# Optimization experiments

Measured on AMD Instinct MI355X. Metric: run time of the kernel, lower is better.

Reference implementation:

```python
import jax, jax.numpy as jnp
import numpy as np
import math

B, S, DM, L = 4, 512, 768, 2
DI, DS, K = 2 * DM, 16, 4          # mamba_ssm defaults: expand=2, d_state=16, d_conv=4
DTR = math.ceil(DM / 16)           # dt_rank = 48
F = 1


def setup_inputs() -> dict:
    key = jax.random.key(0)
    ks = iter(jax.random.split(key, 16))
    g = lambda shape, s=0.02: jax.random.normal(next(ks), shape, jnp.float32) * s
    # sinusoidal positional encoding (precomputed buffer)
    pos = np.arange(S)[:, None].astype(np.float32)
    div = np.exp(np.arange(0, DM, 2).astype(np.float32) * (-math.log(10000.0) / DM))
    pe = np.zeros((S, DM), np.float32)
    pe[:, 0::2] = np.sin(pos * div)
    pe[:, 1::2] = np.cos(pos * div)
    # S4D-real style A init
    A_log = jnp.broadcast_to(jnp.log(jnp.arange(1, DS + 1, dtype=jnp.float32)), (L, DI, DS))
    return dict(
        x=jax.random.normal(next(ks), (B, S, F), jnp.float32),
        w_in=g((DM, F)), b_in=jnp.zeros((DM,), jnp.float32),
        pe=jnp.asarray(pe)[None],                       # (1, S, DM)
        ln1_w=jnp.ones((L, DM)), ln1_b=jnp.zeros((L, DM)),
        w_inproj=g((L, 2 * DI, DM)),
        conv_w=g((L, DI, K), 0.1), conv_b=jnp.zeros((L, DI)),
        w_xproj=g((L, DTR + 2 * DS, DI)),
        w_dt=g((L, DI, DTR)), b_dt=jnp.full((L, DI), -4.0, jnp.float32),
        A_log=A_log, D=jnp.ones((L, DI)),
        w_outproj=g((L, DM, DI)),
        ln2_w=jnp.ones((L, DM)), ln2_b=jnp.zeros((L, DM)),
        ff_w1=g((L, 2 * DM, DM)), ff_b1=jnp.zeros((L, 2 * DM)),
        ff_w2=g((L, DM, 2 * DM)), ff_b2=jnp.zeros((L, DM)),
        lnf_w=jnp.ones((DM,)), lnf_b=jnp.zeros((DM,)),
        w_head=g((1, DM)), b_head=jnp.zeros((1,), jnp.float32),
    )


def _ln(x, w, b):
    mu = x.mean(-1, keepdims=True)
    v = ((x - mu) ** 2).mean(-1, keepdims=True)
    return (x - mu) * jax.lax.rsqrt(v + 1e-5) * w + b


def _mamba(x, w_inproj, conv_w, conv_b, w_xproj, w_dt, b_dt, A_log, D_, w_outproj):
    # x: (B, S, DM)
    Bsz = x.shape[0]
    xz = jnp.einsum('bsd,ed->bse', x, w_inproj)         # (B, S, 2*DI)
    xm, z = jnp.split(xz, 2, axis=-1)
    # causal depthwise conv1d over time
    xc = jax.lax.conv_general_dilated(
        xm.transpose(0, 2, 1), conv_w[:, None, :], (1,), [(K - 1, 0)],
        feature_group_count=DI, dimension_numbers=('NCH', 'OIH', 'NCH'))
    xc = jax.nn.silu((xc + conv_b[:, None]).transpose(0, 2, 1))  # (B, S, DI)
    dbc = jnp.einsum('bsd,ed->bse', xc, w_xproj)        # (B, S, DTR+2*DS)
    dt, Bm, Cm = dbc[..., :DTR], dbc[..., DTR:DTR + DS], dbc[..., DTR + DS:]
    delta = jax.nn.softplus(jnp.einsum('bsr,dr->bsd', dt, w_dt) + b_dt)  # (B, S, DI)
    A = -jnp.exp(A_log)                                 # (DI, DS)

    def step(h, inp):
        d_t, B_t, C_t, u_t = inp                        # (B,DI),(B,DS),(B,DS),(B,DI)
        h = h * jnp.exp(d_t[:, :, None] * A) + (d_t * u_t)[:, :, None] * B_t[:, None, :]
        return h, jnp.einsum('bds,bs->bd', h, C_t)

    h0 = jnp.zeros((Bsz, DI, DS), x.dtype)
    _, ys = jax.lax.scan(step, h0, (delta.transpose(1, 0, 2), Bm.transpose(1, 0, 2),
                                    Cm.transpose(1, 0, 2), xc.transpose(1, 0, 2)))
    y = ys.transpose(1, 0, 2) + xc * D_
    y = y * jax.nn.silu(z)
    return jnp.einsum('bsd,ed->bse', y, w_outproj)


def reference(x, w_in, b_in, pe, ln1_w, ln1_b, w_inproj, conv_w, conv_b, w_xproj,
              w_dt, b_dt, A_log, D, w_outproj, ln2_w, ln2_b, ff_w1, ff_b1,
              ff_w2, ff_b2, lnf_w, lnf_b, w_head, b_head):
    h = jnp.einsum('bsf,df->bsd', x, w_in) + b_in
    h = h + pe[:, :h.shape[1]]
    for l in range(L):  # fixed small layer count
        h = h + _mamba(_ln(h, ln1_w[l], ln1_b[l]), w_inproj[l], conv_w[l], conv_b[l],
                       w_xproj[l], w_dt[l], b_dt[l], A_log[l], D[l], w_outproj[l])
        f = _ln(h, ln2_w[l], ln2_b[l])
        f = jax.nn.gelu(jnp.einsum('bsd,ed->bse', f, ff_w1[l]) + ff_b1[l], approximate=False)
        h = h + jnp.einsum('bse,de->bsd', f, ff_w2[l]) + ff_b2[l]
    h = _ln(h, lnf_w, lnf_b)
    h = h.mean(axis=1)                                  # mean pool over time
    return jnp.einsum('bd,od->bo', h, w_head) + b_head
```

## Files before the change

kernel.cpp:

```cpp
#include <hip/hip_runtime.h>
#include <hip/hip_bf16.h>
#include <math.h>

#define B_ 4
#define S_ 512
#define DM_ 768
#define L_ 2
#define DI_ 1536
#define DS_ 16
#define KC_ 4
#define DTR_ 48
#define NSEG 8
#define TS 64

typedef __hip_bfloat16 bf16;
typedef __attribute__((ext_vector_type(8))) short short8;
typedef __attribute__((ext_vector_type(4))) float f32x4;

#define GLDS16(g, l) __builtin_amdgcn_global_load_lds( \
    (const __attribute__((address_space(1))) void*)(g), \
    (__attribute__((address_space(3))) void*)(l), 16, 0, 0)


__global__ void k_embed(const float* __restrict__ x, const float* __restrict__ w_in,
                        const float* __restrict__ b_in, const float* __restrict__ pe,
                        float* __restrict__ h) {
  int idx = blockIdx.x * 256 + threadIdx.x;
  if (idx >= B_ * S_ * DM_) return;
  int d = idx % DM_;
  int t = idx / DM_;
  int s = t % S_;
  h[idx] = x[t] * w_in[d] + b_in[d] + pe[s * DM_ + d];
}

__global__ void k_ln(const float* __restrict__ in, const float* __restrict__ w,
                     const float* __restrict__ b, bf16* __restrict__ out) {
  __shared__ float red1[4], red2[4];
  __shared__ float s_mu, s_rstd;
  int row = blockIdx.x;
  const float* x = in + (size_t)row * DM_;
  float s1 = 0.f, s2 = 0.f;
  for (int i = threadIdx.x; i < DM_; i += 256) { float v = x[i]; s1 += v; s2 += v * v; }
  for (int off = 32; off; off >>= 1) { s1 += __shfl_down(s1, off); s2 += __shfl_down(s2, off); }
  if ((threadIdx.x & 63) == 0) { red1[threadIdx.x >> 6] = s1; red2[threadIdx.x >> 6] = s2; }
  __syncthreads();
  if (threadIdx.x == 0) {
    float t1 = red1[0] + red1[1] + red1[2] + red1[3];
    float t2 = red2[0] + red2[1] + red2[2] + red2[3];
    float mu = t1 * (1.f / DM_);
    float var = t2 * (1.f / DM_) - mu * mu;
    s_mu = mu;
    s_rstd = rsqrtf(var + 1e-5f);
  }
  __syncthreads();
  float mu = s_mu, rstd = s_rstd;
  for (int i = threadIdx.x; i < DM_; i += 256)
    out[(size_t)row * DM_ + i] = __float2bfloat16((x[i] - mu) * rstd * w[i] + b[i]);
}

__global__ __launch_bounds__(256)
void k_lnred(const float* __restrict__ pxp, int KS,
             const float* __restrict__ hin, const float* __restrict__ bias,
             const float* __restrict__ lw, const float* __restrict__ lb,
             float* __restrict__ hout, bf16* __restrict__ xout) {
  __shared__ float red1[4], red2[4];
  __shared__ float s_mu, s_rstd;
  int row = blockIdx.x;
  float v[3];
  float s1 = 0.f, s2 = 0.f;
#pragma unroll
  for (int j = 0; j < 3; ++j) {
    int n = threadIdx.x + j * 256;
    float s = hin[(size_t)row * DM_ + n];
    if (bias) s += bias[n];
    for (int ks = 0; ks < KS; ++ks)
      s += pxp[(size_t)ks * 2048 * DM_ + (size_t)row * DM_ + n];
    v[j] = s;
    s1 += s; s2 += s * s;
  }
  for (int off = 32; off; off >>= 1) { s1 += __shfl_down(s1, off); s2 += __shfl_down(s2, off); }
  if ((threadIdx.x & 63) == 0) { red1[threadIdx.x >> 6] = s1; red2[threadIdx.x >> 6] = s2; }
  __syncthreads();
  if (threadIdx.x == 0) {
    float t1 = red1[0] + red1[1] + red1[2] + red1[3];
    float t2 = red2[0] + red2[1] + red2[2] + red2[3];
    float mu = t1 * (1.f / DM_);
    float var = t2 * (1.f / DM_) - mu * mu;
    s_mu = mu;
    s_rstd = rsqrtf(var + 1e-5f);
  }
  __syncthreads();
  float mu = s_mu, rstd = s_rstd;
#pragma unroll
  for (int j = 0; j < 3; ++j) {
    int n = threadIdx.x + j * 256;
    hout[(size_t)row * DM_ + n] = v[j];
    xout[(size_t)row * DM_ + n] = __float2bfloat16((v[j] - mu) * rstd * lw[n] + lb[n]);
  }
}

__global__ void k_gelred(const float* __restrict__ pxp, const float* __restrict__ bias,
                         bf16* __restrict__ out) {
  int idx = blockIdx.x * 256 + threadIdx.x;
  if (idx >= 2048 * 2 * DM_) return;
  int n = idx % (2 * DM_);
  float s = pxp[idx] + pxp[(size_t)2048 * 2 * DM_ + idx] + bias[n];
  s = 0.5f * s * (1.f + erff(s * 0.70710678118654752f));
  out[idx] = __float2bfloat16(s);
}

__global__ void k_castall(const float* __restrict__ w_inproj, const float* __restrict__ w_outproj,
                          const float* __restrict__ ff_w1, const float* __restrict__ ff_w2,
                          const float* __restrict__ w_xproj, const float* __restrict__ w_dt,
                          const float* __restrict__ A_log,
                          bf16* __restrict__ wip, bf16* __restrict__ wop,
                          bf16* __restrict__ wf1, bf16* __restrict__ wf2,
                          bf16* __restrict__ wxp, bf16* __restrict__ wdtp,
                          float* __restrict__ At) {
  const int N0 = L_ * 2 * DI_ * DM_;
  const int N1 = L_ * DM_ * DI_;
  const int N2 = L_ * 2 * DM_ * DM_;
  const int N3 = L_ * DM_ * 2 * DM_;
  const int N4 = L_ * 128 * DI_;
  const int N5 = L_ * DI_ * 64;
  const int N6 = L_ * 16 * DI_;
  const int TOT = N0 + N1 + N2 + N3 + N4 + N5 + N6;
  for (int i = blockIdx.x * 256 + threadIdx.x; i < TOT; i += gridDim.x * 256) {
    int j = i;
    if (j < N0) { wip[j] = __float2bfloat16(w_inproj[j]); continue; }
    j -= N0;
    if (j < N1) { wop[j] = __float2bfloat16(w_outproj[j]); continue; }
    j -= N1;
    if (j < N2) { wf1[j] = __float2bfloat16(ff_w1[j]); continue; }
    j -= N2;
    if (j < N3) { wf2[j] = __float2bfloat16(ff_w2[j]); continue; }
    j -= N3;
    if (j < N4) {
      int col = j % DI_;
      int row = (j / DI_) & 127;
      int l = j / (128 * DI_);
      float v = (row < 80) ? w_xproj[((size_t)l * 80 + row) * DI_ + col] : 0.f;
      wxp[j] = __float2bfloat16(v);
      continue;
    }
    j -= N4;
    if (j < N5) {
      int col = j & 63;
      int r = (j >> 6) % DI_;
      int l = j / (DI_ * 64);
      float v = (col < 48) ? w_dt[((size_t)l * DI_ + r) * 48 + col] : 0.f;
      wdtp[j] = __float2bfloat16(v);
      continue;
    }
    j -= N5;
    {
      int d = j % DI_;
      int n = (j / DI_) & 15;
      int l = j / (16 * DI_);
      At[j] = -__expf(A_log[((size_t)l * DI_ + d) * 16 + n]);
    }
  }
}

__global__ void k_conv_silu(const float* __restrict__ xz, const float* __restrict__ cw,
                            const float* __restrict__ cb, float* __restrict__ xc,
                            bf16* __restrict__ xcb) {
  int idx = blockIdx.x * 256 + threadIdx.x;
  if (idx >= B_ * S_ * DI_) return;
  int d = idx % DI_;
  int t = idx / DI_;
  int s = t % S_;
  int b = t / S_;
  float acc = cb[d];
  const float* base = xz + (size_t)(b * S_) * (2 * DI_) + d;
#pragma unroll
  for (int k = 0; k < KC_; ++k) {
    int ss = s - (KC_ - 1) + k;
    if (ss >= 0) acc = fmaf(base[(size_t)ss * (2 * DI_)], cw[d * KC_ + k], acc);
  }
  float v = acc / (1.f + expf(-acc));
  xc[idx] = v;
  xcb[idx] = __float2bfloat16(v);
}

__global__ __launch_bounds__(256)
void k_scanA(const float* __restrict__ delta, const float* __restrict__ xc,
             const float* __restrict__ bc, const float* __restrict__ At,
             const float* __restrict__ Dv,
             float* __restrict__ ylocal, float* __restrict__ cumd,
             float* __restrict__ hend) {
  int b = blockIdx.y;
  int seg = blockIdx.z;
  int d = blockIdx.x * 256 + threadIdx.x;
  int s0 = seg * TS;

  float A[16], hst[16];
#pragma unroll
  for (int n = 0; n < 16; ++n) {
    A[n] = At[(size_t)n * DI_ + d];
    hst[n] = 0.f;
  }
  float Dd = Dv[d];
  float cd = 0.f;

  const float* dp = delta + ((size_t)(b * S_ + s0)) * DI_ + d;
  const float* up = xc + ((size_t)(b * S_ + s0)) * DI_ + d;
  const float* bp = bc + ((size_t)(b * S_ + s0)) * 32;
  float* yp = ylocal + ((size_t)(b * S_ + s0)) * DI_ + d;
  float* cp = cumd + ((size_t)(b * S_ + s0)) * DI_ + d;

  float dl_next = dp[0];
  float u_next = up[0];
#pragma unroll 4
  for (int s = 0; s < TS; ++s) {
    float dl = dl_next, u = u_next;
    if (s + 1 < TS) {
      dl_next = dp[(size_t)(s + 1) * DI_];
      u_next = up[(size_t)(s + 1) * DI_];
    }
    cd += dl;
    float dlu = dl * u;
    float y = 0.f;
#pragma unroll
    for (int n = 0; n < 16; ++n) {
      float e = __expf(dl * A[n]);
      hst[n] = fmaf(hst[n], e, dlu * bp[s * 32 + n]);
      y = fmaf(hst[n], bp[s * 32 + 16 + n], y);
    }
    yp[(size_t)s * DI_] = fmaf(u, Dd, y);
    cp[(size_t)s * DI_] = cd;
  }
  float* hp = hend + ((size_t)(b * NSEG + seg) * 16) * DI_ + d;
#pragma unroll
  for (int n = 0; n < 16; ++n) hp[(size_t)n * DI_] = hst[n];
}

__global__ void k_scanB(const float* __restrict__ hend, const float* __restrict__ cumd,
                        const float* __restrict__ At, float* __restrict__ h0seg) {
  int idx = blockIdx.x * 256 + threadIdx.x;
  if (idx >= B_ * 16 * DI_) return;
  int d = idx % DI_;
  int r = idx / DI_;
  int n = r & 15;
  int b = r >> 4;
  float A = At[(size_t)n * DI_ + d];
  float h0 = 0.f;
  for (int seg = 0; seg < NSEG; ++seg) {
    size_t o = ((size_t)(b * NSEG + seg) * 16 + n) * DI_ + d;
    h0seg[o] = h0;
    float cdt = cumd[((size_t)(b * S_ + seg * TS + TS - 1)) * DI_ + d];
    h0 = h0 * __expf(A * cdt) + hend[o];
  }
}

__global__ __launch_bounds__(256)
void k_scanC(const float* __restrict__ ylocal, const float* __restrict__ cumd,
             const float* __restrict__ bc, const float* __restrict__ At,
             const float* __restrict__ h0seg, const float* __restrict__ xz,
             bf16* __restrict__ yb16) {
  int d = blockIdx.x * 256 + threadIdx.x;
  int t = blockIdx.y;
  int b = blockIdx.z;
  int seg = t / TS;
  size_t o = ((size_t)(b * S_ + t)) * DI_ + d;
  float y = ylocal[o];
  if (seg) {
    float cd = cumd[o];
    const float* Cp = bc + ((size_t)(b * S_ + t)) * 32 + 16;
    const float* Hb = h0seg + ((size_t)(b * NSEG + seg) * 16) * DI_ + d;
#pragma unroll
    for (int n = 0; n < 16; ++n)
      y += Cp[n] * __expf(At[(size_t)n * DI_ + d] * cd) * Hb[(size_t)n * DI_];
  }
  float z = xz[((size_t)(b * S_ + t)) * (2 * DI_) + DI_ + d];
  float sig = 1.f / (1.f + __expf(-z));
  yb16[o] = __float2bfloat16(y * (z * sig));
}

__global__ void k_head1(const bf16* __restrict__ hf, const float* __restrict__ wh,
                        float* __restrict__ partial) {
  __shared__ float red[4];
  int b = blockIdx.y, j = blockIdx.x;
  const bf16* base = hf + ((size_t)b * S_ + j * 32) * DM_;
  float acc = 0.f;
  for (int i = threadIdx.x; i < 32 * DM_; i += 256) {
    int dd = i - (i / DM_) * DM_;
    acc += __bfloat162float(base[i]) * wh[dd];
  }
  for (int off = 32; off; off >>= 1) acc += __shfl_down(acc, off);
  if ((threadIdx.x & 63) == 0) red[threadIdx.x >> 6] = acc;
  __syncthreads();
  if (threadIdx.x == 0)
    partial[b * 16 + j] = red[0] + red[1] + red[2] + red[3];
}

__global__ void k_head2(const float* __restrict__ partial, const float* __restrict__ bh,
                        float* __restrict__ out) {
  int b = threadIdx.x;
  if (b < B_) {
    float acc = 0.f;
    for (int j = 0; j < 16; ++j) acc += partial[b * 16 + j];
    out[b] = acc * (1.f / S_) + bh[0];
  }
}

template <int EPI>
__global__ __launch_bounds__(256)
void k_gemm_mfma(const bf16* __restrict__ A, int lda,
                 const bf16* __restrict__ W, int ldw,
                 const float* __restrict__ bias,
                 void* __restrict__ out1,
                 int ldc, int N, int Kdim, int pmn) {
  __shared__ short As[2][8192];
  __shared__ short Bs[2][8192];

  int nwg = gridDim.x * gridDim.y;
  int orig = blockIdx.y * gridDim.x + blockIdx.x;
  int wg = (nwg % 8 == 0) ? ((orig & 7) * (nwg >> 3) + (orig >> 3)) : orig;
  int m0 = (wg / gridDim.x) * 128;
  int n0 = (wg % gridDim.x) * 128;

  int lane = threadIdx.x & 63;
  int wid = threadIdx.x >> 6;
  int wm = wid >> 1, wn = wid & 1;
  int lr = lane & 15;
  int ch = lane >> 4;
  int koff = blockIdx.z * Kdim;

  f32x4 acc[4][4];
#pragma unroll
  for (int i = 0; i < 4; ++i)
#pragma unroll
    for (int j = 0; j < 4; ++j) {
      acc[i][j][0] = 0.f; acc[i][j][1] = 0.f; acc[i][j][2] = 0.f; acc[i][j][3] = 0.f;
    }

#define GSTAGE(bb, kt)                                                            \
  {                                                                               \
    int k0 = koff + (kt) * 64;                                                    \
    _Pragma("unroll")                                                             \
    for (int c0 = 0; c0 < 4; ++c0) {                                              \
      int c = c0 * 256 + (int)threadIdx.x;                                        \
      int row = c & 127, chk = c >> 7;                                            \
      GLDS16(A + (size_t)(m0 + row) * lda + k0 + chk * 8,                         \
             (char*)&As[bb][0] + c * 16);                                         \
      GLDS16(W + (size_t)(n0 + row) * ldw + k0 + chk * 8,                         \
             (char*)&Bs[bb][0] + c * 16);                                         \
    }                                                                             \
  }

  int nt = Kdim / 64;
  GSTAGE(0, 0);

  for (int t = 0; t < nt; ++t) {
    int buf = t & 1;
    if (t + 1 < nt) {
      GSTAGE(buf ^ 1, t + 1);
      asm volatile("s_waitcnt vmcnt(8)" ::: "memory");
    } else {
      asm volatile("s_waitcnt vmcnt(0)" ::: "memory");
    }
    __builtin_amdgcn_s_barrier();
    __builtin_amdgcn_sched_barrier(0);

    short8 a0[4], a1[4], b0[4], b1[4];
#pragma unroll
    for (int f = 0; f < 4; ++f) {
      a0[f] = *(const short8*)&As[buf][(ch * 128 + wm * 64 + f * 16 + lr) * 8];
      a1[f] = *(const short8*)&As[buf][((4 + ch) * 128 + wm * 64 + f * 16 + lr) * 8];
      b0[f] = *(const short8*)&Bs[buf][(ch * 128 + wn * 64 + f * 16 + lr) * 8];
      b1[f] = *(const short8*)&Bs[buf][((4 + ch) * 128 + wn * 64 + f * 16 + lr) * 8];
    }
    asm volatile("s_waitcnt lgkmcnt(0)" ::: "memory");
    __builtin_amdgcn_sched_barrier(0);
    __builtin_amdgcn_s_setprio(1);
#pragma unroll
    for (int i = 0; i < 4; ++i)
#pragma unroll
      for (int j = 0; j < 4; ++j) {
        acc[i][j] = __builtin_amdgcn_mfma_f32_16x16x32_bf16(a0[i], b0[j], acc[i][j], 0, 0, 0);
        acc[i][j] = __builtin_amdgcn_mfma_f32_16x16x32_bf16(a1[i], b1[j], acc[i][j], 0, 0, 0);
      }
    __builtin_amdgcn_s_setprio(0);
    __builtin_amdgcn_sched_barrier(0);
    __builtin_amdgcn_s_barrier();
  }
#undef GSTAGE

#pragma unroll
  for (int i = 0; i < 4; ++i) {
#pragma unroll
    for (int j = 0; j < 4; ++j) {
      int nl = wn * 64 + j * 16 + (lane & 15);
      int n = n0 + nl;
#pragma unroll
      for (int q = 0; q < 4; ++q) {
        int m = m0 + wm * 64 + i * 16 + (lane >> 4) * 4 + q;
        float v = acc[i][j][q];
        if (EPI == 0) {
          ((float*)out1)[(size_t)m * ldc + n] = v;
        } else if (EPI == 3) {
          v += bias[n];
          v = (v > 20.f) ? v : log1pf(expf(v));
          ((float*)out1)[(size_t)m * ldc + n] = v;
        } else if (EPI == 5) {
          ((float*)out1)[(size_t)blockIdx.z * pmn + (size_t)m * N + n] = v;
        }
      }
    }
  }
}

__global__ void k_xreduce(const float* __restrict__ pxp, bf16* __restrict__ dtp,
                          float* __restrict__ bcb) {
  int idx = blockIdx.x * 256 + threadIdx.x;
  if (idx >= 2048 * 128) return;
  int m = idx >> 7, n = idx & 127;
  float s = 0.f;
#pragma unroll
  for (int k = 0; k < 8; ++k) s += pxp[(size_t)k * 2048 * 128 + idx];
  if (n < 64) dtp[m * 64 + n] = __float2bfloat16(n < 48 ? s : 0.f);
  if (n >= 48 && n < 80) bcb[m * 32 + (n - 48)] = s;
}


extern "C" void kernel_launch(void* const* d_in, const int* in_sizes, int n_in,
                              void* d_out, int out_size, void* d_ws, size_t ws_size,
                              hipStream_t stream) {
  const float* x        = (const float*)d_in[0];
  const float* w_in     = (const float*)d_in[1];
  const float* b_in     = (const float*)d_in[2];
  const float* pe       = (const float*)d_in[3];
  const float* ln1_w    = (const float*)d_in[4];
  const float* ln1_b    = (const float*)d_in[5];
  const float* w_inproj = (const float*)d_in[6];
  const float* conv_w   = (const float*)d_in[7];
  const float* conv_b   = (const float*)d_in[8];
  const float* w_xproj  = (const float*)d_in[9];
  const float* w_dt     = (const float*)d_in[10];
  const float* b_dt     = (const float*)d_in[11];
  const float* A_log    = (const float*)d_in[12];
  const float* Dv       = (const float*)d_in[13];
  const float* w_outproj= (const float*)d_in[14];
  const float* ln2_w    = (const float*)d_in[15];
  const float* ln2_b    = (const float*)d_in[16];
  const float* ff_w1    = (const float*)d_in[17];
  const float* ff_b1    = (const float*)d_in[18];
  const float* ff_w2    = (const float*)d_in[19];
  const float* ff_b2    = (const float*)d_in[20];
  const float* lnf_w    = (const float*)d_in[21];
  const float* lnf_b    = (const float*)d_in[22];
  const float* w_head   = (const float*)d_in[23];
  const float* b_head   = (const float*)d_in[24];
  float* out = (float*)d_out;

  const int M = B_ * S_;

  float* wsf = (float*)d_ws;
  float* h    = wsf; wsf += (size_t)M * DM_;
  float* xz   = wsf; wsf += (size_t)M * 2 * DI_;
  float* xc   = wsf; wsf += (size_t)M * DI_;
  float* bc   = wsf; wsf += (size_t)M * 32;
  float* dlt  = wsf; wsf += (size_t)M * DI_;
  float* hend = wsf; wsf += (size_t)B_ * NSEG * DI_ * 16;
  float* h0sg = wsf; wsf += (size_t)B_ * NSEG * DI_ * 16;
  float* pxp  = wsf; wsf += (size_t)4 * M * 2 * DM_;
  float* At   = wsf; wsf += (size_t)L_ * 16 * DI_;
  float* part = wsf; wsf += 64;
  bf16* wsb = (bf16*)wsf;
  bf16* xln16 = wsb; wsb += (size_t)M * DM_;
  bf16* xcb   = wsb; wsb += (size_t)M * DI_;
  bf16* dtp   = wsb; wsb += (size_t)M * 64;
  bf16* yb16  = wsb; wsb += (size_t)M * DI_;
  bf16* ffh16 = wsb; wsb += (size_t)M * DI_;
  bf16* wip   = wsb; wsb += (size_t)L_ * 2 * DI_ * DM_;
  bf16* wxp   = wsb; wsb += (size_t)L_ * 128 * DI_;
  bf16* wdtp  = wsb; wsb += (size_t)L_ * DI_ * 64;
  bf16* wop   = wsb; wsb += (size_t)L_ * DM_ * DI_;
  bf16* wf1   = wsb; wsb += (size_t)L_ * 2 * DM_ * DM_;
  bf16* wf2   = wsb; wsb += (size_t)L_ * DM_ * 2 * DM_;

  float* ylocal = dlt;
  float* cumd   = xc;

  dim3 blk(256);

  k_castall<<<2048, blk, 0, stream>>>(w_inproj, w_outproj, ff_w1, ff_w2,
                                      w_xproj, w_dt, A_log,
                                      wip, wop, wf1, wf2, wxp, wdtp, At);

  k_embed<<<(B_ * S_ * DM_ + 255) / 256, blk, 0, stream>>>(x, w_in, b_in, pe, h);
  k_ln<<<M, blk, 0, stream>>>(h, ln1_w, ln1_b, xln16);

  for (int l = 0; l < L_; ++l) {
    const float* Atl = At + (size_t)l * 16 * DI_;

    k_gemm_mfma<0><<<dim3(2 * DI_ / 128, M / 128), blk, 0, stream>>>(
        xln16, DM_, wip + (size_t)l * 2 * DI_ * DM_, DM_, nullptr,
        xz, 2 * DI_, 2 * DI_, DM_, 0);

    k_conv_silu<<<(B_ * S_ * DI_ + 255) / 256, blk, 0, stream>>>(
        xz, conv_w + l * DI_ * KC_, conv_b + l * DI_, xc, xcb);

    k_gemm_mfma<5><<<dim3(1, M / 128, 8), blk, 0, stream>>>(
        xcb, DI_, wxp + (size_t)l * 128 * DI_, DI_, nullptr,
        pxp, 128, 128, DI_ / 8, M * 128);
    k_xreduce<<<(M * 128) / 256, blk, 0, stream>>>(pxp, dtp, bc);

    k_gemm_mfma<3><<<dim3(DI_ / 128, M / 128), blk, 0, stream>>>(
        dtp, 64, wdtp + (size_t)l * DI_ * 64, 64, b_dt + l * DI_,
        dlt, DI_, DI_, 64, 0);

    k_scanA<<<dim3(DI_ / 256, B_, NSEG), blk, 0, stream>>>(
        dlt, xc, bc, Atl, Dv + l * DI_, ylocal, cumd, hend);
    k_scanB<<<(B_ * 16 * DI_ + 255) / 256, blk, 0, stream>>>(hend, cumd, Atl, h0sg);
    k_scanC<<<dim3(DI_ / 256, S_, B_), blk, 0, stream>>>(
        ylocal, cumd, bc, Atl, h0sg, xz, yb16);

    k_gemm_mfma<5><<<dim3(DM_ / 128, M / 128, 4), blk, 0, stream>>>(
        yb16, DI_, wop + (size_t)l * DM_ * DI_, DI_, nullptr,
        pxp, DM_, DM_, DI_ / 4, M * DM_);
    k_lnred<<<M, blk, 0, stream>>>(pxp, 4, h, nullptr,
                                   ln2_w + l * DM_, ln2_b + l * DM_, h, xln16);

    k_gemm_mfma<5><<<dim3(2 * DM_ / 128, M / 128, 2), blk, 0, stream>>>(
        xln16, DM_, wf1 + (size_t)l * 2 * DM_ * DM_, DM_, nullptr,
        pxp, 2 * DM_, 2 * DM_, DM_ / 2, M * 2 * DM_);
    k_gelred<<<(M * 2 * DM_) / 256, blk, 0, stream>>>(pxp, ff_b1 + l * 2 * DM_, ffh16);

    k_gemm_mfma<5><<<dim3(DM_ / 128, M / 128, 4), blk, 0, stream>>>(
        ffh16, 2 * DM_, wf2 + (size_t)l * DM_ * 2 * DM_, 2 * DM_, nullptr,
        pxp, DM_, DM_, DI_ / 4, M * DM_);
    const float* nlw = (l + 1 < L_) ? ln1_w + (l + 1) * DM_ : lnf_w;
    const float* nlb = (l + 1 < L_) ? ln1_b + (l + 1) * DM_ : lnf_b;
    k_lnred<<<M, blk, 0, stream>>>(pxp, 4, h, ff_b2 + l * DM_, nlw, nlb, h, xln16);
  }

  k_head1<<<dim3(16, B_), blk, 0, stream>>>(xln16, w_head, part);
  k_head2<<<1, 64, 0, stream>>>(part, b_head, out);
}
```

Measured before the change: 539.7 us.

## Store in-proj output as bf16, fuse embed+LN, and use finer scan segments

The in-projection GEMM now writes its output in bf16 through a new epilogue, and the conv and gating kernels read that bf16 buffer, which halves the traffic for the largest intermediate. The embedding and first LayerNorm are merged into a single per-row kernel, removing one launch and a round trip through memory. The chunked scan now uses 32 segments of 16 steps instead of 8 of 64, which gives more parallelism in the local scan at the cost of a longer sequential carry pass. Rounding xz to bf16 adds precision loss in the conv input and the z gate.

```diff
diff --git a/kernel.cpp b/kernel.cpp
--- a/kernel.cpp
+++ b/kernel.cpp
@@ -10,8 +10,8 @@
 #define DS_ 16
 #define KC_ 4
 #define DTR_ 48
-#define NSEG 8
-#define TS 64
+#define NSEG 32
+#define TS 16
 
 typedef __hip_bfloat16 bf16;
 typedef __attribute__((ext_vector_type(8))) short short8;
@@ -22,25 +22,25 @@
     (__attribute__((address_space(3))) void*)(l), 16, 0, 0)
 
 
-__global__ void k_embed(const float* __restrict__ x, const float* __restrict__ w_in,
-                        const float* __restrict__ b_in, const float* __restrict__ pe,
-                        float* __restrict__ h) {
-  int idx = blockIdx.x * 256 + threadIdx.x;
-  if (idx >= B_ * S_ * DM_) return;
-  int d = idx % DM_;
-  int t = idx / DM_;
-  int s = t % S_;
-  h[idx] = x[t] * w_in[d] + b_in[d] + pe[s * DM_ + d];
-}
-
-__global__ void k_ln(const float* __restrict__ in, const float* __restrict__ w,
-                     const float* __restrict__ b, bf16* __restrict__ out) {
+__global__ __launch_bounds__(256)
+void k_embed_ln(const float* __restrict__ x, const float* __restrict__ w_in,
+                const float* __restrict__ b_in, const float* __restrict__ pe,
+                const float* __restrict__ lw, const float* __restrict__ lb,
+                float* __restrict__ h, bf16* __restrict__ xout) {
   __shared__ float red1[4], red2[4];
   __shared__ float s_mu, s_rstd;
   int row = blockIdx.x;
-  const float* x = in + (size_t)row * DM_;
+  int s = row % S_;
+  float xv = x[row];
+  float v[3];
   float s1 = 0.f, s2 = 0.f;
-  for (int i = threadIdx.x; i < DM_; i += 256) { float v = x[i]; s1 += v; s2 += v * v; }
+#pragma unroll
+  for (int j = 0; j < 3; ++j) {
+    int d = threadIdx.x + j * 256;
+    float t = xv * w_in[d] + b_in[d] + pe[s * DM_ + d];
+    v[j] = t;
+    s1 += t; s2 += t * t;
+  }
   for (int off = 32; off; off >>= 1) { s1 += __shfl_down(s1, off); s2 += __shfl_down(s2, off); }
   if ((threadIdx.x & 63) == 0) { red1[threadIdx.x >> 6] = s1; red2[threadIdx.x >> 6] = s2; }
   __syncthreads();
@@ -54,8 +54,12 @@
   }
   __syncthreads();
   float mu = s_mu, rstd = s_rstd;
-  for (int i = threadIdx.x; i < DM_; i += 256)
-    out[(size_t)row * DM_ + i] = __float2bfloat16((x[i] - mu) * rstd * w[i] + b[i]);
+#pragma unroll
+  for (int j = 0; j < 3; ++j) {
+    int d = threadIdx.x + j * 256;
+    h[(size_t)row * DM_ + d] = v[j];
+    xout[(size_t)row * DM_ + d] = __float2bfloat16((v[j] - mu) * rstd * lw[d] + lb[d]);
+  }
 }
 
 __global__ __launch_bounds__(256)
@@ -162,7 +166,7 @@
   }
 }
 
-__global__ void k_conv_silu(const float* __restrict__ xz, const float* __restrict__ cw,
+__global__ void k_conv_silu(const bf16* __restrict__ xz, const float* __restrict__ cw,
                             const float* __restrict__ cb, float* __restrict__ xc,
                             bf16* __restrict__ xcb) {
   int idx = blockIdx.x * 256 + threadIdx.x;
@@ -172,11 +176,11 @@
   int s = t % S_;
   int b = t / S_;
   float acc = cb[d];
-  const float* base = xz + (size_t)(b * S_) * (2 * DI_) + d;
+  const bf16* base = xz + (size_t)(b * S_) * (2 * DI_) + d;
 #pragma unroll
   for (int k = 0; k < KC_; ++k) {
     int ss = s - (KC_ - 1) + k;
-    if (ss >= 0) acc = fmaf(base[(size_t)ss * (2 * DI_)], cw[d * KC_ + k], acc);
+    if (ss >= 0) acc = fmaf(__bfloat162float(base[(size_t)ss * (2 * DI_)]), cw[d * KC_ + k], acc);
   }
   float v = acc / (1.f + expf(-acc));
   xc[idx] = v;
@@ -256,7 +260,7 @@
 __global__ __launch_bounds__(256)
 void k_scanC(const float* __restrict__ ylocal, const float* __restrict__ cumd,
              const float* __restrict__ bc, const float* __restrict__ At,
-             const float* __restrict__ h0seg, const float* __restrict__ xz,
+             const float* __restrict__ h0seg, const bf16* __restrict__ xz,
              bf16* __restrict__ yb16) {
   int d = blockIdx.x * 256 + threadIdx.x;
   int t = blockIdx.y;
@@ -272,7 +276,7 @@
     for (int n = 0; n < 16; ++n)
       y += Cp[n] * __expf(At[(size_t)n * DI_ + d] * cd) * Hb[(size_t)n * DI_];
   }
-  float z = xz[((size_t)(b * S_ + t)) * (2 * DI_) + DI_ + d];
+  float z = __bfloat162float(xz[((size_t)(b * S_ + t)) * (2 * DI_) + DI_ + d]);
   float sig = 1.f / (1.f + __expf(-z));
   yb16[o] = __float2bfloat16(y * (z * sig));
 }
@@ -405,6 +409,8 @@
           ((float*)out1)[(size_t)m * ldc + n] = v;
         } else if (EPI == 5) {
           ((float*)out1)[(size_t)blockIdx.z * pmn + (size_t)m * N + n] = v;
+        } else if (EPI == 6) {
+          ((bf16*)out1)[(size_t)m * ldc + n] = __float2bfloat16(v);
         }
       }
     }
@@ -458,7 +464,6 @@
 
   float* wsf = (float*)d_ws;
   float* h    = wsf; wsf += (size_t)M * DM_;
-  float* xz   = wsf; wsf += (size_t)M * 2 * DI_;
   float* xc   = wsf; wsf += (size_t)M * DI_;
   float* bc   = wsf; wsf += (size_t)M * 32;
   float* dlt  = wsf; wsf += (size_t)M * DI_;
@@ -469,6 +474,7 @@
   float* part = wsf; wsf += 64;
   bf16* wsb = (bf16*)wsf;
   bf16* xln16 = wsb; wsb += (size_t)M * DM_;
+  bf16* xz16  = wsb; wsb += (size_t)M * 2 * DI_;
   bf16* xcb   = wsb; wsb += (size_t)M * DI_;
   bf16* dtp   = wsb; wsb += (size_t)M * 64;
   bf16* yb16  = wsb; wsb += (size_t)M * DI_;
@@ -489,18 +495,17 @@
                                       w_xproj, w_dt, A_log,
                                       wip, wop, wf1, wf2, wxp, wdtp, At);
 
-  k_embed<<<(B_ * S_ * DM_ + 255) / 256, blk, 0, stream>>>(x, w_in, b_in, pe, h);
-  k_ln<<<M, blk, 0, stream>>>(h, ln1_w, ln1_b, xln16);
+  k_embed_ln<<<M, blk, 0, stream>>>(x, w_in, b_in, pe, ln1_w, ln1_b, h, xln16);
 
   for (int l = 0; l < L_; ++l) {
     const float* Atl = At + (size_t)l * 16 * DI_;
 
-    k_gemm_mfma<0><<<dim3(2 * DI_ / 128, M / 128), blk, 0, stream>>>(
+    k_gemm_mfma<6><<<dim3(2 * DI_ / 128, M / 128), blk, 0, stream>>>(
         xln16, DM_, wip + (size_t)l * 2 * DI_ * DM_, DM_, nullptr,
-        xz, 2 * DI_, 2 * DI_, DM_, 0);
+        xz16, 2 * DI_, 2 * DI_, DM_, 0);
 
     k_conv_silu<<<(B_ * S_ * DI_ + 255) / 256, blk, 0, stream>>>(
-        xz, conv_w + l * DI_ * KC_, conv_b + l * DI_, xc, xcb);
+        xz16, conv_w + l * DI_ * KC_, conv_b + l * DI_, xc, xcb);
 
     k_gemm_mfma<5><<<dim3(1, M / 128, 8), blk, 0, stream>>>(
         xcb, DI_, wxp + (size_t)l * 128 * DI_, DI_, nullptr,
@@ -515,7 +520,7 @@
         dlt, xc, bc, Atl, Dv + l * DI_, ylocal, cumd, hend);
     k_scanB<<<(B_ * 16 * DI_ + 255) / 256, blk, 0, stream>>>(hend, cumd, Atl, h0sg);
     k_scanC<<<dim3(DI_ / 256, S_, B_), blk, 0, stream>>>(
-        ylocal, cumd, bc, Atl, h0sg, xz, yb16);
+        ylocal, cumd, bc, Atl, h0sg, xz16, yb16);
 
     k_gemm_mfma<5><<<dim3(DM_ / 128, M / 128, 4), blk, 0, stream>>>(
         yb16, DI_, wop + (size_t)l * DM_ * DI_, DI_, nullptr,
```

New measurement: 492.6 us. -8.7%, faster.
